# Performance work log

Hardware: AMD Instinct MI355X
Metric: run time of the kernel (lower is better)

## Reference

```python
import jax, jax.numpy as jnp
import numpy as np

N_EMBD = 2048
N_HEAD = 16
KV_GROUP = 4
HEAD_DIM = N_EMBD // N_HEAD          # 128
N_KV = N_HEAD // KV_GROUP            # 4
KV_DIM = N_KV * HEAD_DIM             # 512
B, T = 2, 2048
ROPE_THETA = 1000000.0


def setup_inputs() -> dict:
    key = jax.random.key(0)
    k0, k1, k2 = jax.random.split(key, 3)
    x = jax.random.normal(k0, (B, T, N_EMBD), dtype=jnp.float32)
    # weights stored (in, out); matches torch Linear math up to a transpose of random init
    W_attn = jax.random.normal(k1, (N_EMBD, N_EMBD + 2 * KV_DIM), dtype=jnp.float32) * 0.02
    b_attn = jnp.zeros((N_EMBD + 2 * KV_DIM,), dtype=jnp.float32)
    W_proj = jax.random.normal(k2, (N_EMBD, N_EMBD), dtype=jnp.float32) * 0.02
    # realistic RoPE frequencies (Qwen-style theta)
    inv_freq = 1.0 / (ROPE_THETA ** (np.arange(0, HEAD_DIM, 2, dtype=np.float64) / HEAD_DIM))
    ang = np.outer(np.arange(T, dtype=np.float64), inv_freq)  # (T, HEAD_DIM//2)
    freqs_cos = jnp.asarray(np.cos(ang), dtype=jnp.float32)
    freqs_sin = jnp.asarray(np.sin(ang), dtype=jnp.float32)
    return {"x": x, "W_attn": W_attn, "b_attn": b_attn, "W_proj": W_proj,
            "freqs_cos": freqs_cos, "freqs_sin": freqs_sin}


def _rope_expand(x, cos, sin, kv_group):
    # x: (B, T, n_kv, hd); complex rotate interleaved pairs, then expand to n_kv*kv_group heads
    Bx, Tx, nh, hd = x.shape
    xf = x.astype(jnp.float32).reshape(Bx, Tx, nh, hd // 2, 2)
    a, b = xf[..., 0], xf[..., 1]
    c = cos[None, :, None, :]  # (1, T, 1, hd//2)
    s = sin[None, :, None, :]
    yr = a * c - b * s
    yi = a * s + b * c
    y = jnp.stack([yr, yi], axis=-1).reshape(Bx, Tx, nh, hd)
    y = jnp.broadcast_to(y[:, :, :, None, :], (Bx, Tx, nh, kv_group, hd))
    return y.reshape(Bx, Tx, nh * kv_group, hd).astype(x.dtype)


def reference(x, W_attn, b_attn, W_proj, freqs_cos, freqs_sin):
    Bx, Tx, E = x.shape
    hd = 2 * freqs_cos.shape[-1]
    n_q = E // hd
    kv_dim = (W_attn.shape[1] - E) // 2
    n_kv = kv_dim // hd
    g = n_q // n_kv

    qkv = x @ W_attn + b_attn  # (B, T, E + 2*kv_dim)
    q = qkv[..., :E].reshape(Bx, Tx, n_q, hd).transpose(0, 2, 1, 3)          # bhtd
    k = qkv[..., E:E + kv_dim].reshape(Bx, Tx, n_kv, hd)
    v = qkv[..., E + kv_dim:].reshape(Bx, Tx, n_kv, hd)
    # faithful to source: RoPE on K AND V (not Q), then GQA expand
    k = _rope_expand(k, freqs_cos, freqs_sin, g).transpose(0, 2, 1, 3)       # bhtd
    v = _rope_expand(v, freqs_cos, freqs_sin, g).transpose(0, 2, 1, 3)       # bhtd

    scale = 1.0 / jnp.sqrt(jnp.asarray(hd, dtype=x.dtype))
    scores = jnp.einsum('bhqd,bhkd->bhqk', q, k) * scale                     # (B, H, T, T)
    causal = jnp.tril(jnp.ones((Tx, Tx), dtype=bool))
    scores = jnp.where(causal, scores, jnp.asarray(-jnp.inf, scores.dtype))
    attn = jax.nn.softmax(scores, axis=-1)
    y = jnp.einsum('bhqk,bhkd->bhqd', attn, v)
    y = y.transpose(0, 2, 1, 3).reshape(Bx, Tx, E)
    return y @ W_proj  # c_proj, no bias
```

## Files before the change

kernel.cpp:

```cpp
#include <hip/hip_runtime.h>
#include <cstdint>
#include <cstddef>

#define T_SEQ 2048
#define B_SZ  2
#define EMB   2048
#define NH    16
#define NKV   4
#define HD    128
#define KVD   512
#define QKVN  3072
#define MROWS (B_SZ*T_SEQ)

typedef __bf16 bf16x8 __attribute__((ext_vector_type(8)));
typedef float  f32x4  __attribute__((ext_vector_type(4)));
typedef short  s16x8  __attribute__((ext_vector_type(8)));
typedef unsigned short u16;

__device__ __forceinline__ u16 f2b(float f) {
  uint32_t u = __builtin_bit_cast(uint32_t, f);
  u += 0x7fffu + ((u >> 16) & 1u);
  return (u16)(u >> 16);
}
__device__ __forceinline__ float b2f(u16 h) {
  return __builtin_bit_cast(float, (uint32_t)h << 16);
}
__device__ __forceinline__ bf16x8 ld_bf8(const u16* p) {
  return __builtin_bit_cast(bf16x8, *(const s16x8*)p);
}
__device__ __forceinline__ void glds16(const void* g, void* l) {
  __builtin_amdgcn_global_load_lds((const __attribute__((address_space(1))) void*)g,
                                   (__attribute__((address_space(3))) void*)l, 16, 0, 0);
}
template<int N> __device__ __forceinline__ void waitv() {
  if constexpr (N == 0) asm volatile("s_waitcnt vmcnt(0)" ::: "memory");
  else if constexpr (N == 2) asm volatile("s_waitcnt vmcnt(2)" ::: "memory");
  else if constexpr (N == 3) asm volatile("s_waitcnt vmcnt(3)" ::: "memory");
  __builtin_amdgcn_sched_barrier(0);
}

__global__ void cvt_x_kernel(const float4* __restrict__ x, ushort4* __restrict__ xb, int n4) {
  int i = blockIdx.x*blockDim.x + threadIdx.x;
  if (i >= n4) return;
  float4 v = x[i];
  ushort4 o;
  o.x = f2b(v.x); o.y = f2b(v.y); o.z = f2b(v.z); o.w = f2b(v.w);
  xb[i] = o;
}

__global__ void transpose_w_kernel(const float* __restrict__ in, u16* __restrict__ out,
                                   int R, int C) {
  __shared__ float tile[32][33];
  int c0 = blockIdx.x*32, r0 = blockIdx.y*32;
  int tx = threadIdx.x, ty = threadIdx.y;
#pragma unroll
  for (int i = 0; i < 32; i += 8)
    tile[ty+i][tx] = in[(size_t)(r0+ty+i)*C + c0+tx];
  __syncthreads();
#pragma unroll
  for (int i = 0; i < 32; i += 8)
    out[(size_t)(c0+ty+i)*R + r0+tx] = f2b(tile[tx][ty+i]);
}

template<int BN, int WGN, int MF, int NF, int NF1, int SB, int SB1, int VMC, bool BF16_OUT>
__global__ __launch_bounds__(512, 2) void gemm_kernel(const u16* __restrict__ A,
        const u16* __restrict__ Bt, const float* __restrict__ bias,
        void* __restrict__ Cout, int M, int N, int K) {
  constexpr int MF2 = MF/2;
  __shared__ u16 As[2][256*64];
  __shared__ u16 Bs[2][BN*64];
  const int tid = threadIdx.x;
  const int w = tid >> 6, lane = tid & 63;
  const int quad = lane >> 4, lc = lane & 15;
  const int wrow = w / WGN, wcol = w % WGN;
  const int gx = gridDim.x;
  const int lin = blockIdx.y*gx + blockIdx.x;
  const int swz = (lin & 7)*32 + (lin >> 3);
  const int m0 = (swz / gx)*256, n0 = (swz % gx)*BN;

  f32x4 acc[MF][NF] = {};
  bf16x8 af[MF2][2], bfv[NF][2];

  int xoff[2];
#pragma unroll
  for (int ks = 0; ks < 2; ++ks) xoff[ks] = ((ks*4 + quad) ^ (lc & 7))*8;
  const int arow0 = (wrow*MF*16 + lc)*64;
  const int brow0 = (wcol*NF*16 + lc)*64;

  const int srb  = tid >> 3;
  const int spos = (tid & 7) ^ (srb & 7);
  const u16* sAp = A  + (size_t)(m0 + srb)*K + spos*8;
  const u16* sBp = Bt + (size_t)(n0 + srb)*K + spos*8;

#define STAGE_A(bf_, t_, h_) do { \
    glds16(sAp + (size_t)((h_)*2  )*64*K + (size_t)(t_)*64, &As[bf_][((h_)*2  )*4096 + w*512]); \
    glds16(sAp + (size_t)((h_)*2+1)*64*K + (size_t)(t_)*64, &As[bf_][((h_)*2+1)*4096 + w*512]); \
  } while (0)
#define STAGE_B(bf_, t_, p_) do { \
    _Pragma("unroll") for (int r = (p_) ? SB1 : 0; r < ((p_) ? SB : SB1); ++r) \
      glds16(sBp + (size_t)r*64*K + (size_t)(t_)*64, &Bs[bf_][r*4096 + w*512]); \
  } while (0)
#define LDAH(S_, h_) do { _Pragma("unroll") for (int i = 0; i < MF2; ++i) { \
    af[i][0] = ld_bf8((S_) + arow0 + ((h_)*MF2 + i)*1024 + xoff[0]); \
    af[i][1] = ld_bf8((S_) + arow0 + ((h_)*MF2 + i)*1024 + xoff[1]); } } while (0)
#define LDBG(S_, g_) do { _Pragma("unroll") for (int j = (g_) ? NF1 : 0; j < ((g_) ? NF : NF1); ++j) { \
    bfv[j][0] = ld_bf8((S_) + brow0 + j*1024 + xoff[0]); \
    bfv[j][1] = ld_bf8((S_) + brow0 + j*1024 + xoff[1]); } } while (0)
#define CL(h_, g_) do { _Pragma("unroll") for (int ks = 0; ks < 2; ++ks) \
    _Pragma("unroll") for (int i = 0; i < MF2; ++i) \
    _Pragma("unroll") for (int j = (g_) ? NF1 : 0; j < ((g_) ? NF : NF1); ++j) \
      acc[(h_)*MF2+i][j] = __builtin_amdgcn_mfma_f32_16x16x32_bf16( \
          af[i][ks], bfv[j][ks], acc[(h_)*MF2+i][j], 0, 0, 0); } while (0)
#define BARX()  __builtin_amdgcn_s_barrier()
#define SCHB()  __builtin_amdgcn_sched_barrier(0)
#define MFMAPH(h_, g_) do { BARX(); \
    asm volatile("s_waitcnt lgkmcnt(0)" ::: "memory"); SCHB(); \
    __builtin_amdgcn_s_setprio(1); CL(h_, g_); __builtin_amdgcn_s_setprio(0); \
  } while (0)

  const int NT = K >> 6;
  STAGE_B(0, 0, 0); STAGE_B(0, 0, 1);
  STAGE_A(0, 0, 0); STAGE_A(0, 0, 1);
  STAGE_B(1, 1, 0); STAGE_B(1, 1, 1);
  waitv<VMC>();
  BARX(); SCHB();

  for (int t0 = 0; t0 < NT-2; t0 += 2) {
    const u16 *a0 = As[0], *b0 = Bs[0], *a1 = As[1], *b1 = Bs[1];
    LDAH(a0, 0); LDBG(b0, 0); STAGE_A(1, t0+1, 0);
    MFMAPH(0, 0); BARX();
    LDBG(b0, 1); STAGE_A(1, t0+1, 1);
    MFMAPH(0, 1); BARX();
    LDAH(a0, 1); STAGE_B(0, t0+2, 0);
    MFMAPH(1, 0); BARX();
    STAGE_B(0, t0+2, 1);
    MFMAPH(1, 1);
    waitv<VMC>();
    BARX(); SCHB();
    LDAH(a1, 0); LDBG(b1, 0); STAGE_A(0, t0+2, 0);
    MFMAPH(0, 0); BARX();
    LDBG(b1, 1); STAGE_A(0, t0+2, 1);
    MFMAPH(0, 1); BARX();
    LDAH(a1, 1); STAGE_B(1, t0+3, 0);
    MFMAPH(1, 0); BARX();
    STAGE_B(1, t0+3, 1);
    MFMAPH(1, 1);
    waitv<VMC>();
    BARX(); SCHB();
  }
  {
    const u16 *a0 = As[0], *b0 = Bs[0], *a1 = As[1], *b1 = Bs[1];
    LDAH(a0, 0); LDBG(b0, 0); STAGE_A(1, NT-1, 0);
    MFMAPH(0, 0); BARX();
    LDBG(b0, 1); STAGE_A(1, NT-1, 1);
    MFMAPH(0, 1); BARX();
    LDAH(a0, 1);
    MFMAPH(1, 0); BARX();
    MFMAPH(1, 1);
    waitv<0>();
    BARX(); SCHB();
    LDAH(a1, 0); LDBG(b1, 0);
    MFMAPH(0, 0); BARX();
    LDBG(b1, 1);
    MFMAPH(0, 1); BARX();
    LDAH(a1, 1);
    MFMAPH(1, 0); BARX();
    MFMAPH(1, 1);
  }

#undef STAGE_A
#undef STAGE_B
#undef LDAH
#undef LDBG
#undef CL
#undef BARX
#undef SCHB
#undef MFMAPH

#pragma unroll
  for (int j = 0; j < NF; ++j) {
    int col = n0 + wcol*NF*16 + j*16 + lc;
    float bv = BF16_OUT ? bias[col] : 0.0f;
#pragma unroll
    for (int i = 0; i < MF; ++i) {
      int rowb = m0 + wrow*MF*16 + i*16 + quad*4;
#pragma unroll
      for (int r = 0; r < 4; ++r) {
        float v = acc[i][j][r] + bv;
        if (BF16_OUT) ((u16*)Cout)[(size_t)(rowb+r)*N + col] = f2b(v);
        else          ((float*)Cout)[(size_t)(rowb+r)*N + col] = v;
      }
    }
  }
}

__global__ void rope_kernel(const u16* __restrict__ qkv, const float* __restrict__ fc,
                            const float* __restrict__ fs, u16* __restrict__ kout,
                            u16* __restrict__ vout) {
  int tid = threadIdx.x;
  int row = blockIdx.x;
  int i = tid & 63, kv = tid >> 6;
  int t = row & (T_SEQ-1);
  const u16* p = qkv + (size_t)row*QKVN + EMB + kv*HD + 2*i;
  float ka = b2f(p[0]),   kb = b2f(p[1]);
  float va = b2f(p[KVD]), vb = b2f(p[KVD+1]);
  float c = fc[t*64+i], s = fs[t*64+i];
  size_t ob = (size_t)row*KVD + kv*HD + 2*i;
  kout[ob]   = f2b(ka*c - kb*s);
  kout[ob+1] = f2b(ka*s + kb*c);
  vout[ob]   = f2b(va*c - vb*s);
  vout[ob+1] = f2b(va*s + vb*c);
}

__global__ void transpose_v_kernel(const u16* __restrict__ vb, u16* __restrict__ vtb) {
  __shared__ u16 tile[32][33];
  int bkv = blockIdx.z;
  int b = bkv >> 2, kv = bkv & 3;
  int d0 = blockIdx.y*32, t0 = blockIdx.x*32;
  int tx = threadIdx.x, ty = threadIdx.y;
#pragma unroll
  for (int i = 0; i < 32; i += 8)
    tile[ty+i][tx] = vb[(size_t)(b*T_SEQ + t0+ty+i)*KVD + kv*HD + d0 + tx];
  __syncthreads();
#pragma unroll
  for (int i = 0; i < 32; i += 8)
    vtb[(size_t)(bkv*HD + d0+ty+i)*T_SEQ + t0 + tx] = tile[tx][ty+i];
}

__global__ __launch_bounds__(256, 2) void flash_kernel(const u16* __restrict__ qkv,
    const u16* __restrict__ kb, const u16* __restrict__ vtb, u16* __restrict__ yb) {
  constexpr int PP = 72;
  __shared__ u16 Ks[2][64*128];
  __shared__ u16 Vs[2][128*64];
  __shared__ u16 Ps[4][16*PP];
  const int tid = threadIdx.x;
  const int w = tid >> 6, lane = tid & 63;
  const int quad = lane >> 4, lc = lane & 15;
  const int bkv = blockIdx.x & 7;
  const int r_  = blockIdx.x >> 3;
  const int b = bkv >> 2, kv = bkv & 3;
  const int h = kv*4 + w;
  const int qbase = (127 - r_)*16;

  bf16x8 qf[4];
  {
    const u16* qp = qkv + (size_t)(b*T_SEQ + qbase + lc)*QKVN + h*HD + quad*8;
#pragma unroll
    for (int ks = 0; ks < 4; ++ks) qf[ks] = ld_bf8(qp + ks*32);
  }

  f32x4 o[8] = {};
  float rs[4] = {0.f, 0.f, 0.f, 0.f};
  const u16* kbase = kb  + (size_t)b*T_SEQ*KVD + kv*HD;
  const u16* vbase = vtb + (size_t)bkv*HD*T_SEQ;
  const int nk = qbase + 16;
  const int nt = (nk + 63) >> 6;
  const float cs = 0.08838834764831845f * 1.4426950408889634f;
  u16* pw = Ps[w];

  const u16* kptr[4];
  const u16* vptr[4];
#pragma unroll
  for (int rr = 0; rr < 4; ++rr) {
    int krow = (rr*4 + w)*4 + (lane >> 4);
    int kcc  = (lane & 15) ^ (krow & 15);
    kptr[rr] = kbase + (size_t)krow*KVD + kcc*8;
    int vrow = (rr*4 + w)*8 + (lane >> 3);
    int vcc  = (lane & 7) ^ (vrow & 7);
    vptr[rr] = vbase + (size_t)vrow*T_SEQ + vcc*8;
  }

  int koff[4], voff[2];
#pragma unroll
  for (int ks = 0; ks < 4; ++ks) koff[ks] = lc*128 + (((ks*4 + quad) ^ lc)*8);
#pragma unroll
  for (int ks = 0; ks < 2; ++ks) voff[ks] = lc*64 + (((ks*4 + quad) ^ (lc & 7))*8);

#pragma unroll
  for (int rr = 0; rr < 4; ++rr) glds16(kptr[rr], &Ks[0][(rr*4 + w)*512]);
#pragma unroll
  for (int rr = 0; rr < 4; ++rr) glds16(vptr[rr], &Vs[0][(rr*4 + w)*512]);
  asm volatile("s_waitcnt vmcnt(0)" ::: "memory");
  __builtin_amdgcn_sched_barrier(0);
  __builtin_amdgcn_s_barrier();
  __builtin_amdgcn_sched_barrier(0);

  for (int t = 0; t < nt; ++t) {
    const int cur = t & 1;
    if (t + 1 < nt) {
#pragma unroll
      for (int rr = 0; rr < 4; ++rr)
        glds16(kptr[rr] + (size_t)(t+1)*64*KVD, &Ks[cur^1][(rr*4 + w)*512]);
#pragma unroll
      for (int rr = 0; rr < 4; ++rr)
        glds16(vptr[rr] + (size_t)(t+1)*64,     &Vs[cur^1][(rr*4 + w)*512]);
    }
    const u16* ksb = Ks[cur];
    const u16* vsb = Vs[cur];
    const int k0 = t*64;

    f32x4 sc[4] = {};
    __builtin_amdgcn_s_setprio(1);
#pragma unroll
    for (int nt2 = 0; nt2 < 4; ++nt2)
#pragma unroll
      for (int ks = 0; ks < 4; ++ks) {
        bf16x8 kf = ld_bf8(ksb + nt2*16*128 + koff[ks]);
        sc[nt2] = __builtin_amdgcn_mfma_f32_16x16x32_bf16(qf[ks], kf, sc[nt2], 0, 0, 0);
      }
    __builtin_amdgcn_s_setprio(0);

    if (k0 + 63 > qbase) {
#pragma unroll
      for (int nt2 = 0; nt2 < 4; ++nt2) {
        int key = k0 + nt2*16 + lc;
        int qrow = qbase + quad*4;
#pragma unroll
        for (int r = 0; r < 4; ++r) {
          float e = __builtin_amdgcn_exp2f(sc[nt2][r]*cs);
          float p = (key <= qrow + r) ? e : 0.0f;
          rs[r] += p;
          pw[(quad*4 + r)*PP + nt2*16 + lc] = f2b(p);
        }
      }
    } else {
#pragma unroll
      for (int nt2 = 0; nt2 < 4; ++nt2)
#pragma unroll
        for (int r = 0; r < 4; ++r) {
          float p = __builtin_amdgcn_exp2f(sc[nt2][r]*cs);
          rs[r] += p;
          pw[(quad*4 + r)*PP + nt2*16 + lc] = f2b(p);
        }
    }

    bf16x8 pa[2];
#pragma unroll
    for (int ks = 0; ks < 2; ++ks)
      pa[ks] = ld_bf8(pw + lc*PP + ks*32 + quad*8);

    __builtin_amdgcn_s_setprio(1);
#pragma unroll
    for (int j = 0; j < 8; ++j)
#pragma unroll
      for (int ks = 0; ks < 2; ++ks) {
        bf16x8 vf = ld_bf8(vsb + j*16*64 + voff[ks]);
        o[j] = __builtin_amdgcn_mfma_f32_16x16x32_bf16(pa[ks], vf, o[j], 0, 0, 0);
      }
    __builtin_amdgcn_s_setprio(0);

    asm volatile("s_waitcnt vmcnt(0)" ::: "memory");
    __builtin_amdgcn_sched_barrier(0);
    __builtin_amdgcn_s_barrier();
    __builtin_amdgcn_sched_barrier(0);
  }

#pragma unroll
  for (int r = 0; r < 4; ++r) {
    float v = rs[r];
#pragma unroll
    for (int off2 = 8; off2 >= 1; off2 >>= 1)
      v += __shfl_xor(v, off2);
    float inv = 1.0f / v;
    size_t orow = (size_t)(b*T_SEQ + qbase + quad*4 + r)*EMB + h*HD;
#pragma unroll
    for (int j = 0; j < 8; ++j)
      yb[orow + j*16 + lc] = f2b(o[j][r]*inv);
  }
}

extern "C" void kernel_launch(void* const* d_in, const int* in_sizes, int n_in,
                              void* d_out, int out_size, void* d_ws, size_t ws_size,
                              hipStream_t stream) {
  const float* x      = (const float*)d_in[0];
  const float* W_attn = (const float*)d_in[1];
  const float* b_attn = (const float*)d_in[2];
  const float* W_proj = (const float*)d_in[3];
  const float* fc     = (const float*)d_in[4];
  const float* fs     = (const float*)d_in[5];

  u16* ws   = (u16*)d_ws;
  u16* xb   = ws;
  u16* WaT  = xb   + (size_t)MROWS*EMB;
  u16* qkv  = WaT  + (size_t)QKVN*EMB;
  u16* kbuf = qkv  + (size_t)MROWS*QKVN;
  u16* vb   = kbuf + (size_t)MROWS*KVD;
  u16* vtb  = vb   + (size_t)MROWS*KVD;
  u16* WpT  = WaT;
  u16* yb   = xb;
  float* out = (float*)d_out;

  cvt_x_kernel<<<(MROWS*EMB/4 + 255)/256, 256, 0, stream>>>(
      (const float4*)x, (ushort4*)xb, MROWS*EMB/4);
  transpose_w_kernel<<<dim3(QKVN/32, EMB/32), dim3(32, 8), 0, stream>>>(
      W_attn, WaT, EMB, QKVN);
  gemm_kernel<192, 4, 8, 3, 2, 3, 2, 3, true>
      <<<dim3(QKVN/192, MROWS/256), 512, 0, stream>>>(
      xb, WaT, b_attn, qkv, MROWS, QKVN, EMB);
  rope_kernel<<<MROWS, 256, 0, stream>>>(qkv, fc, fs, kbuf, vb);
  transpose_v_kernel<<<dim3(T_SEQ/32, HD/32, B_SZ*NKV), dim3(32, 8), 0, stream>>>(vb, vtb);
  transpose_w_kernel<<<dim3(EMB/32, EMB/32), dim3(32, 8), 0, stream>>>(
      W_proj, WpT, EMB, EMB);
  flash_kernel<<<dim3(B_SZ*NKV*(T_SEQ/16)), 256, 0, stream>>>(qkv, kbuf, vtb, yb);
  gemm_kernel<128, 2, 4, 4, 2, 2, 1, 2, false>
      <<<dim3(EMB/128, MROWS/256), 512, 0, stream>>>(
      yb, WpT, nullptr, out, MROWS, EMB, EMB);
}
```

Measured before the change: 281.4 us.

## Vectorize weight transpose with 64x64 tiles and XOR-swizzle flash P buffer

The weight transpose kernel now works on 64x64 tiles, loading float4 and storing ushort4 per thread instead of scalars, which cuts the number of global memory transactions. Separately, the per-wave P staging buffer in the flash kernel drops its padded pitch of 72. It uses a 64-wide layout with an XOR swizzle on 8-element chunks, applied to both the scalar writes and the vector reads, to avoid LDS bank conflicts without padding. The transpose's column reads from the 65-pitch tile may still conflict, and the swizzle adds some index arithmetic.

New measurement: 283.1 us. No clear change (+0.6%).

```diff
diff --git a/kernel.cpp b/kernel.cpp
--- a/kernel.cpp
+++ b/kernel.cpp
@@ -50,16 +50,27 @@
 
 __global__ void transpose_w_kernel(const float* __restrict__ in, u16* __restrict__ out,
                                    int R, int C) {
-  __shared__ float tile[32][33];
-  int c0 = blockIdx.x*32, r0 = blockIdx.y*32;
+  __shared__ float tile[64][65];
+  int c0 = blockIdx.x*64, r0 = blockIdx.y*64;
   int tx = threadIdx.x, ty = threadIdx.y;
 #pragma unroll
-  for (int i = 0; i < 32; i += 8)
-    tile[ty+i][tx] = in[(size_t)(r0+ty+i)*C + c0+tx];
+  for (int k = 0; k < 4; ++k) {
+    int r = ty + k*16;
+    float4 v = *(const float4*)&in[(size_t)(r0+r)*C + c0 + tx*4];
+    tile[r][tx*4+0] = v.x; tile[r][tx*4+1] = v.y;
+    tile[r][tx*4+2] = v.z; tile[r][tx*4+3] = v.w;
+  }
   __syncthreads();
 #pragma unroll
-  for (int i = 0; i < 32; i += 8)
-    out[(size_t)(c0+ty+i)*R + r0+tx] = f2b(tile[tx][ty+i]);
+  for (int k = 0; k < 4; ++k) {
+    int c = ty + k*16;
+    ushort4 o;
+    o.x = f2b(tile[tx*4+0][c]);
+    o.y = f2b(tile[tx*4+1][c]);
+    o.z = f2b(tile[tx*4+2][c]);
+    o.w = f2b(tile[tx*4+3][c]);
+    *(ushort4*)&out[(size_t)(c0+c)*R + r0 + tx*4] = o;
+  }
 }
 
 template<int BN, int WGN, int MF, int NF, int NF1, int SB, int SB1, int VMC, bool BF16_OUT>
@@ -229,10 +240,9 @@
 
 __global__ __launch_bounds__(256, 2) void flash_kernel(const u16* __restrict__ qkv,
     const u16* __restrict__ kb, const u16* __restrict__ vtb, u16* __restrict__ yb) {
-  constexpr int PP = 72;
   __shared__ u16 Ks[2][64*128];
   __shared__ u16 Vs[2][128*64];
-  __shared__ u16 Ps[4][16*PP];
+  __shared__ u16 Ps[4][16*64];
   const int tid = threadIdx.x;
   const int w = tid >> 6, lane = tid & 63;
   const int quad = lane >> 4, lc = lane & 15;
@@ -270,11 +280,20 @@
     vptr[rr] = vbase + (size_t)vrow*T_SEQ + vcc*8;
   }
 
-  int koff[4], voff[2];
+  int koff[4], voff[2], poff[2];
 #pragma unroll
   for (int ks = 0; ks < 4; ++ks) koff[ks] = lc*128 + (((ks*4 + quad) ^ lc)*8);
 #pragma unroll
   for (int ks = 0; ks < 2; ++ks) voff[ks] = lc*64 + (((ks*4 + quad) ^ (lc & 7))*8);
+#pragma unroll
+  for (int ks = 0; ks < 2; ++ks) poff[ks] = lc*64 + (((ks*4 + quad) ^ (lc & 7))*8);
+  int pwb[4], pwx[4];
+#pragma unroll
+  for (int r = 0; r < 4; ++r) {
+    pwb[r] = (quad*4 + r)*64 + (lc & 7);
+    pwx[r] = (quad*4 + r) & 7;
+  }
+  const int pcc = lc >> 3;
 
 #pragma unroll
   for (int rr = 0; rr < 4; ++rr) glds16(kptr[rr], &Ks[0][(rr*4 + w)*512]);
@@ -320,7 +339,7 @@
           float e = __builtin_amdgcn_exp2f(sc[nt2][r]*cs);
           float p = (key <= qrow + r) ? e : 0.0f;
           rs[r] += p;
-          pw[(quad*4 + r)*PP + nt2*16 + lc] = f2b(p);
+          pw[pwb[r] + ((nt2*2 + pcc) ^ pwx[r])*8] = f2b(p);
         }
       }
     } else {
@@ -330,14 +349,14 @@
         for (int r = 0; r < 4; ++r) {
           float p = __builtin_amdgcn_exp2f(sc[nt2][r]*cs);
           rs[r] += p;
-          pw[(quad*4 + r)*PP + nt2*16 + lc] = f2b(p);
+          pw[pwb[r] + ((nt2*2 + pcc) ^ pwx[r])*8] = f2b(p);
         }
     }
 
     bf16x8 pa[2];
 #pragma unroll
     for (int ks = 0; ks < 2; ++ks)
-      pa[ks] = ld_bf8(pw + lc*PP + ks*32 + quad*8);
+      pa[ks] = ld_bf8(pw + poff[ks]);
 
     __builtin_amdgcn_s_setprio(1);
 #pragma unroll
@@ -392,14 +411,14 @@
 
   cvt_x_kernel<<<(MROWS*EMB/4 + 255)/256, 256, 0, stream>>>(
       (const float4*)x, (ushort4*)xb, MROWS*EMB/4);
-  transpose_w_kernel<<<dim3(QKVN/32, EMB/32), dim3(32, 8), 0, stream>>>(
+  transpose_w_kernel<<<dim3(QKVN/64, EMB/64), dim3(16, 16), 0, stream>>>(
       W_attn, WaT, EMB, QKVN);
   gemm_kernel<192, 4, 8, 3, 2, 3, 2, 3, true>
       <<<dim3(QKVN/192, MROWS/256), 512, 0, stream>>>(
       xb, WaT, b_attn, qkv, MROWS, QKVN, EMB);
   rope_kernel<<<MROWS, 256, 0, stream>>>(qkv, fc, fs, kbuf, vb);
   transpose_v_kernel<<<dim3(T_SEQ/32, HD/32, B_SZ*NKV), dim3(32, 8), 0, stream>>>(vb, vtb);
-  transpose_w_kernel<<<dim3(EMB/32, EMB/32), dim3(32, 8), 0, stream>>>(
+  transpose_w_kernel<<<dim3(EMB/64, EMB/64), dim3(16, 16), 0, stream>>>(
       W_proj, WpT, EMB, EMB);
   flash_kernel<<<dim3(B_SZ*NKV*(T_SEQ/16)), 256, 0, stream>>>(qkv, kbuf, vtb, yb);
   gemm_kernel<128, 2, 4, 4, 2, 2, 1, 2, false>
```
